# Performance work log

Hardware: AMD Instinct MI355X
Metric: run time of the kernel (lower is better)

## Reference

```python
import jax, jax.numpy as jnp
import numpy as np

B, D, C = 4096, 4096, 1024


def setup_inputs() -> dict:
    key = jax.random.key(0)
    kx, kw = jax.random.split(key)
    x = jax.random.normal(kx, (B, D), dtype=jnp.float32)
    # kaiming_normal_ with nonlinearity='relu': std = sqrt(2 / fan_in)
    W = jax.random.normal(kw, (C, D), dtype=jnp.float32) * jnp.sqrt(2.0 / D)
    return {"x": x, "W": W}


def reference(x, W):
    # Original: -( (x[:, :, None] - W.T[None, :, :])**2 ).mean(axis=1)
    d = x.shape[1]
    x_sq = jnp.sum(x * x, axis=1, keepdims=True)        # [B, 1]
    w_sq = jnp.sum(W * W, axis=1)[None, :]              # [1, C]
    cross = jnp.einsum('bd,cd->bc', x, W)               # [B, C] tensor-core GEMM
    return -(x_sq - 2.0 * cross + w_sq) / d
```

## Files before the change

### kernel.cpp

```cpp
#include <hip/hip_runtime.h>
#include <hip/hip_bf16.h>


typedef float f32x4 __attribute__((ext_vector_type(4)));
typedef float f32x2 __attribute__((ext_vector_type(2)));
typedef long long2_t __attribute__((ext_vector_type(2)));

#define BDIM 4096
#define DDIM 4096
#define CDIM 1024
#define TM 128
#define TN 128
#define BK 64
#define KSPLIT 4
#define NIT ((DDIM / KSPLIT) / BK)
#define SCALE 32.0f
#define INV_SS (1.0f/1024.0f)
#define PSCALE 0.0625f

#define SYNC_LGKM() asm volatile("s_waitcnt lgkmcnt(0)\n\ts_barrier" ::: "memory")

__global__ __launch_bounds__(256) void cvt_rowsq(
    const float* __restrict__ x, const float* __restrict__ W,
    unsigned char* __restrict__ xb, unsigned char* __restrict__ wb,
    float* __restrict__ xsq, float* __restrict__ wsq)
{
    const int lane = threadIdx.x & 63;
    const int row = blockIdx.x * 4 + (threadIdx.x >> 6);

    const float* src;
    unsigned char* dst;
    float* sq;
    if (row < BDIM) {
        src = x + (size_t)row * DDIM;
        dst = xb + (size_t)row * DDIM;
        sq = xsq + row;
    } else {
        int r = row - BDIM;
        src = W + (size_t)r * DDIM;
        dst = wb + (size_t)r * DDIM;
        sq = wsq + r;
    }

    const float4* s4 = (const float4*)src;
    unsigned int* d4 = (unsigned int*)dst;
    float a = 0.f;
    #pragma unroll
    for (int s = 0; s < DDIM / 4 / 64; ++s) {
        float4 f = s4[lane + 64 * s];
        a += f.x * f.x + f.y * f.y + f.z * f.z + f.w * f.w;
        unsigned int p = 0;
        p = __builtin_amdgcn_cvt_pk_fp8_f32(f.x * SCALE, f.y * SCALE, p, false);
        p = __builtin_amdgcn_cvt_pk_fp8_f32(f.z * SCALE, f.w * SCALE, p, true);
        d4[lane + 64 * s] = p;
    }
    #pragma unroll
    for (int off = 32; off > 0; off >>= 1) a += __shfl_down(a, off);
    if (lane == 0) *sq = a;
}

struct Pref { long2_t a0, a1, b0, b1; };

__global__ __launch_bounds__(256, 3) void gemm_eucl(
    const unsigned char* __restrict__ xb,
    const unsigned char* __restrict__ wb,
    unsigned int* __restrict__ part)
{
    __shared__ unsigned char sm[2 * 16384];

    const int tid = threadIdx.x;
    const int lane = tid & 63;
    const int wid = tid >> 6;
    const int bm = blockIdx.x * TM;
    const int bn = blockIdx.y * TN;
    const int ks = blockIdx.z * (DDIM / KSPLIT);
    const int wm = (wid >> 1) * 64;
    const int wn = (wid & 1) * 64;

    const int r0 = tid >> 2, c = tid & 3;
    const unsigned int oA0 = (unsigned int)((bm + r0) * DDIM + ks + c * 16);
    const unsigned int oA1 = oA0 + 64u * DDIM;
    const unsigned int oB0 = (unsigned int)((bn + r0) * DDIM + ks + c * 16);
    const unsigned int oB1 = oB0 + 64u * DDIM;

    const int k2o = (c >> 1) * 8;
    const int kcw = (c & 1) * 2;
    const int wo0 = r0 * 64 + ((kcw ^ (r0 & 3)) * 16) + k2o;
    const int wo1 = r0 * 64 + (((kcw | 1) ^ (r0 & 3)) * 16) + k2o;

    const int kc = lane >> 4;
    const int ml = lane & 15;
    int aoff[4], boff[4];
    #pragma unroll
    for (int i = 0; i < 4; ++i) {
        int m = wm + i * 16 + ml;
        aoff[i] = m * 64 + ((kc ^ (m & 3)) * 16);
        int n = wn + i * 16 + ml;
        boff[i] = n * 64 + ((kc ^ (n & 3)) * 16);
    }

    f32x4 acc[4][4] = {};

#define LOADSET(S, KT)                                                   \
    do {                                                                 \
        (S).a0 = *(const long2_t*)(xb + oA0 + (KT) * BK);                \
        (S).a1 = *(const long2_t*)(xb + oA1 + (KT) * BK);                \
        (S).b0 = *(const long2_t*)(wb + oB0 + (KT) * BK);                \
        (S).b1 = *(const long2_t*)(wb + oB1 + (KT) * BK);                \
    } while (0)

#define WRITESET(buf, S)                                                 \
    do {                                                                 \
        unsigned char* sA = sm + (buf) * 16384;                          \
        unsigned char* sB = sA + 8192;                                   \
        *(long*)(sA + wo0) = (S).a0.x; *(long*)(sA + wo1) = (S).a0.y;    \
        *(long*)(sA + wo0 + 4096) = (S).a1.x;                            \
        *(long*)(sA + wo1 + 4096) = (S).a1.y;                            \
        *(long*)(sB + wo0) = (S).b0.x; *(long*)(sB + wo1) = (S).b0.y;    \
        *(long*)(sB + wo0 + 4096) = (S).b1.x;                            \
        *(long*)(sB + wo1 + 4096) = (S).b1.y;                            \
    } while (0)

#define MFMA8(LA, I)                                                     \
    do {                                                                 \
        _Pragma("unroll")                                                \
        for (int j = 0; j < 4; ++j) {                                    \
            acc[I][j] = __builtin_amdgcn_mfma_f32_16x16x32_fp8_fp8(      \
                (LA).x, lb[j].x, acc[I][j], 0, 0, 0);                    \
            acc[I][j] = __builtin_amdgcn_mfma_f32_16x16x32_fp8_fp8(      \
                (LA).y, lb[j].y, acc[I][j], 0, 0, 0);                    \
        }                                                                \
    } while (0)

#define COMPUTE(buf)                                                     \
    do {                                                                 \
        const unsigned char* sA = sm + (buf) * 16384;                    \
        const unsigned char* sB = sA + 8192;                             \
        long2_t lb[4];                                                   \
        _Pragma("unroll")                                                \
        for (int j = 0; j < 4; ++j) lb[j] = *(const long2_t*)(sB + boff[j]); \
        long2_t laA = *(const long2_t*)(sA + aoff[0]);                   \
        long2_t laB = *(const long2_t*)(sA + aoff[1]);                   \
        MFMA8(laA, 0);                                                   \
        laA = *(const long2_t*)(sA + aoff[2]);                           \
        MFMA8(laB, 1);                                                   \
        laB = *(const long2_t*)(sA + aoff[3]);                           \
        MFMA8(laA, 2);                                                   \
        MFMA8(laB, 3);                                                   \
    } while (0)

    Pref S[3];
    LOADSET(S[0], 0);
    LOADSET(S[1], 1);
    LOADSET(S[2], 2);
    WRITESET(0, S[0]);
    SYNC_LGKM();

    #pragma unroll
    for (int k = 0; k < NIT - 1; ++k) {
        if (k < NIT - 3) LOADSET(S[k % 3], k + 3);
        COMPUTE(k & 1);
        WRITESET((k + 1) & 1, S[(k + 1) % 3]);
        SYNC_LGKM();
    }
    COMPUTE((NIT - 1) & 1);

    unsigned int* p = part
        + (((size_t)blockIdx.z * 256 + (blockIdx.x * 8 + blockIdx.y)) * 16) * 256;
    #pragma unroll
    for (int i = 0; i < 4; ++i)
        #pragma unroll
        for (int j = 0; j < 4; ++j) {
            unsigned int pk = 0;
            pk = __builtin_amdgcn_cvt_pk_fp8_f32(
                acc[i][j][0] * PSCALE, acc[i][j][1] * PSCALE, pk, false);
            pk = __builtin_amdgcn_cvt_pk_fp8_f32(
                acc[i][j][2] * PSCALE, acc[i][j][3] * PSCALE, pk, true);
            p[(i * 4 + j) * 256 + tid] = pk;
        }
#undef LOADSET
#undef WRITESET
#undef MFMA8
#undef COMPUTE
}

__global__ __launch_bounds__(256) void reduce_out(
    const unsigned int* __restrict__ part, const float* __restrict__ xsq,
    const float* __restrict__ wsq, float* __restrict__ out)
{
    const int bid = blockIdx.x;
    const int bb = bid >> 1;
    const int f0 = (bid & 1) * 8;
    const int t = threadIdx.x;
    const int lane = t & 63;
    const int wid = t >> 6;
    const int bm = (bb >> 3) * TM, bn = (bb & 7) * TN;
    const int wm = (wid >> 1) * 64, wn = (wid & 1) * 64;
    const int row_l = (lane >> 4) * 4, col_l = lane & 15;
    const size_t sl = (size_t)256 * 16 * 256;
    const float c1 = 2.0f * 16.0f * INV_SS / (float)DDIM;
    const float c2 = 1.0f / (float)DDIM;

    #pragma unroll
    for (int f = f0; f < f0 + 8; ++f) {
        size_t o = ((size_t)bb * 16 + f) * 256 + t;
        f32x2 s01 = {0.f, 0.f}, s23 = {0.f, 0.f};
        #pragma unroll
        for (int z = 0; z < KSPLIT; ++z) {
            unsigned int u = part[o + (size_t)z * sl];
            s01 += __builtin_amdgcn_cvt_pk_f32_fp8(u, false);
            s23 += __builtin_amdgcn_cvt_pk_f32_fp8(u, true);
        }
        int i = f >> 2, j = f & 3;
        int gn = bn + wn + j * 16 + col_l;
        float wv = wsq[gn];
        float sv[4] = {s01.x, s01.y, s23.x, s23.y};
        #pragma unroll
        for (int r = 0; r < 4; ++r) {
            int gm = bm + wm + i * 16 + row_l + r;
            out[(size_t)gm * CDIM + gn] = sv[r] * c1 - (xsq[gm] + wv) * c2;
        }
    }
}

__global__ void fallback_kernel(const float* __restrict__ x, const float* __restrict__ W,
                                float* __restrict__ out)
{
    int c = blockIdx.x * blockDim.x + threadIdx.x;
    int b = blockIdx.y;
    if (c >= CDIM) return;
    const float* xr = x + (size_t)b * DDIM;
    const float* wr = W + (size_t)c * DDIM;
    float xs = 0.f, ws = 0.f, cr = 0.f;
    for (int d = 0; d < DDIM; ++d) {
        float xv = xr[d], wv = wr[d];
        xs += xv * xv; ws += wv * wv; cr += xv * wv;
    }
    out[(size_t)b * CDIM + c] = (2.0f * cr - xs - ws) / (float)DDIM;
}

extern "C" void kernel_launch(void* const* d_in, const int* in_sizes, int n_in,
                              void* d_out, int out_size, void* d_ws, size_t ws_size,
                              hipStream_t stream) {
    const float* x = (const float*)d_in[0];
    const float* W = (const float*)d_in[1];
    float* out = (float*)d_out;

    size_t need = (size_t)(BDIM + CDIM) * DDIM
                + (size_t)(BDIM + CDIM) * sizeof(float)
                + (size_t)KSPLIT * BDIM * CDIM;
    if (ws_size < need) {
        fallback_kernel<<<dim3(CDIM / 256, BDIM), 256, 0, stream>>>(x, W, out);
        return;
    }

    unsigned char* xb = (unsigned char*)d_ws;
    unsigned char* wb = xb + (size_t)BDIM * DDIM;
    float* xsq = (float*)(wb + (size_t)CDIM * DDIM);
    float* wsq = xsq + BDIM;
    unsigned int* part = (unsigned int*)(wsq + CDIM);

    cvt_rowsq<<<(BDIM + CDIM) / 4, 256, 0, stream>>>(x, W, xb, wb, xsq, wsq);
    gemm_eucl<<<dim3(BDIM / TM, CDIM / TN, KSPLIT), 256, 0, stream>>>(xb, wb, part);
    reduce_out<<<512, 256, 0, stream>>>(part, xsq, wsq, out);
}
```

Baseline: 144.2 us.

## Switch FP8 GEMM to 32x32x64 scaled MFMA with new LDS swizzle

Replaces the 16x16x32 fp8 MFMA pairs with the MI355X 32x32x64 f8f6f4 scaled MFMA, using unit scales. Each wave now computes four 32x32 tiles. LDS writes become single 16-byte stores under a new XOR swizzle, and fragment reads are paired 16-byte loads. The output layout in the partial buffer changes, and the reduction kernel's index mapping is updated to match. The aim is fewer MFMA issues and LDS instructions per K step, at the cost of possible bank conflicts or register pressure under the new layout.

```diff
diff --git a/kernel.cpp b/kernel.cpp
--- a/kernel.cpp
+++ b/kernel.cpp
@@ -4,7 +4,9 @@
 
 typedef float f32x4 __attribute__((ext_vector_type(4)));
 typedef float f32x2 __attribute__((ext_vector_type(2)));
-typedef long long2_t __attribute__((ext_vector_type(2)));
+typedef float f32x16 __attribute__((ext_vector_type(16)));
+typedef int i32x4 __attribute__((ext_vector_type(4)));
+typedef int i32x8 __attribute__((ext_vector_type(8)));
 
 #define BDIM 4096
 #define DDIM 4096
@@ -59,7 +61,18 @@
     if (lane == 0) *sq = a;
 }
 
-struct Pref { long2_t a0, a1, b0, b1; };
+struct Pref { i32x4 a0, a1, b0, b1; };
+
+__device__ __forceinline__ i32x8 rd8(const unsigned char* p0,
+                                     const unsigned char* p1) {
+    i32x4 lo = *(const i32x4*)p0;
+    i32x4 hi = *(const i32x4*)p1;
+    return __builtin_shufflevector(lo, hi, 0, 1, 2, 3, 4, 5, 6, 7);
+}
+
+#define MXMFMA(A, Bv, C)                                                  \
+    __builtin_amdgcn_mfma_scale_f32_32x32x64_f8f6f4(                      \
+        (A), (Bv), (C), 0, 0, 0, 0x7F7F7F7F, 0, 0x7F7F7F7F)
 
 __global__ __launch_bounds__(256, 3) void gemm_eucl(
     const unsigned char* __restrict__ xb,
@@ -83,70 +96,49 @@
     const unsigned int oB0 = (unsigned int)((bn + r0) * DDIM + ks + c * 16);
     const unsigned int oB1 = oB0 + 64u * DDIM;
 
-    const int k2o = (c >> 1) * 8;
-    const int kcw = (c & 1) * 2;
-    const int wo0 = r0 * 64 + ((kcw ^ (r0 & 3)) * 16) + k2o;
-    const int wo1 = r0 * 64 + (((kcw | 1) ^ (r0 & 3)) * 16) + k2o;
-
-    const int kc = lane >> 4;
-    const int ml = lane & 15;
-    int aoff[4], boff[4];
-    #pragma unroll
-    for (int i = 0; i < 4; ++i) {
-        int m = wm + i * 16 + ml;
-        aoff[i] = m * 64 + ((kc ^ (m & 3)) * 16);
-        int n = wn + i * 16 + ml;
-        boff[i] = n * 64 + ((kc ^ (n & 3)) * 16);
-    }
-
-    f32x4 acc[4][4] = {};
+    const int wo0 = r0 * 64 + ((c ^ ((r0 >> 1) & 3)) * 16);
+
+    const int sswz = (lane >> 1) & 3;
+    const int c0 = (lane >> 5) * 2;
+    const int m0 = wm + (lane & 31);
+    const int n0 = wn + (lane & 31);
+    const int aof0 = m0 * 64 + ((c0 ^ sswz) * 16);
+    const int aof1 = m0 * 64 + (((c0 + 1) ^ sswz) * 16);
+    const int bof0 = n0 * 64 + ((c0 ^ sswz) * 16);
+    const int bof1 = n0 * 64 + (((c0 + 1) ^ sswz) * 16);
+
+    f32x16 acc[4] = {};
 
 #define LOADSET(S, KT)                                                   \
     do {                                                                 \
-        (S).a0 = *(const long2_t*)(xb + oA0 + (KT) * BK);                \
-        (S).a1 = *(const long2_t*)(xb + oA1 + (KT) * BK);                \
-        (S).b0 = *(const long2_t*)(wb + oB0 + (KT) * BK);                \
-        (S).b1 = *(const long2_t*)(wb + oB1 + (KT) * BK);                \
+        (S).a0 = *(const i32x4*)(xb + oA0 + (KT) * BK);                  \
+        (S).a1 = *(const i32x4*)(xb + oA1 + (KT) * BK);                  \
+        (S).b0 = *(const i32x4*)(wb + oB0 + (KT) * BK);                  \
+        (S).b1 = *(const i32x4*)(wb + oB1 + (KT) * BK);                  \
     } while (0)
 
 #define WRITESET(buf, S)                                                 \
     do {                                                                 \
         unsigned char* sA = sm + (buf) * 16384;                          \
         unsigned char* sB = sA + 8192;                                   \
-        *(long*)(sA + wo0) = (S).a0.x; *(long*)(sA + wo1) = (S).a0.y;    \
-        *(long*)(sA + wo0 + 4096) = (S).a1.x;                            \
-        *(long*)(sA + wo1 + 4096) = (S).a1.y;                            \
-        *(long*)(sB + wo0) = (S).b0.x; *(long*)(sB + wo1) = (S).b0.y;    \
-        *(long*)(sB + wo0 + 4096) = (S).b1.x;                            \
-        *(long*)(sB + wo1 + 4096) = (S).b1.y;                            \
-    } while (0)
-
-#define MFMA8(LA, I)                                                     \
-    do {                                                                 \
-        _Pragma("unroll")                                                \
-        for (int j = 0; j < 4; ++j) {                                    \
-            acc[I][j] = __builtin_amdgcn_mfma_f32_16x16x32_fp8_fp8(      \
-                (LA).x, lb[j].x, acc[I][j], 0, 0, 0);                    \
-            acc[I][j] = __builtin_amdgcn_mfma_f32_16x16x32_fp8_fp8(      \
-                (LA).y, lb[j].y, acc[I][j], 0, 0, 0);                    \
-        }                                                                \
+        *(i32x4*)(sA + wo0) = (S).a0;                                    \
+        *(i32x4*)(sA + wo0 + 4096) = (S).a1;                             \
+        *(i32x4*)(sB + wo0) = (S).b0;                                    \
+        *(i32x4*)(sB + wo0 + 4096) = (S).b1;                             \
     } while (0)
 
 #define COMPUTE(buf)                                                     \
     do {                                                                 \
         const unsigned char* sA = sm + (buf) * 16384;                    \
         const unsigned char* sB = sA + 8192;                             \
-        long2_t lb[4];                                                   \
-        _Pragma("unroll")                                                \
-        for (int j = 0; j < 4; ++j) lb[j] = *(const long2_t*)(sB + boff[j]); \
-        long2_t laA = *(const long2_t*)(sA + aoff[0]);                   \
-        long2_t laB = *(const long2_t*)(sA + aoff[1]);                   \
-        MFMA8(laA, 0);                                                   \
-        laA = *(const long2_t*)(sA + aoff[2]);                           \
-        MFMA8(laB, 1);                                                   \
-        laB = *(const long2_t*)(sA + aoff[3]);                           \
-        MFMA8(laA, 2);                                                   \
-        MFMA8(laB, 3);                                                   \
+        i32x8 fb0 = rd8(sB + bof0, sB + bof1);                           \
+        i32x8 fb1 = rd8(sB + bof0 + 2048, sB + bof1 + 2048);             \
+        i32x8 fa0 = rd8(sA + aof0, sA + aof1);                           \
+        acc[0] = MXMFMA(fa0, fb0, acc[0]);                               \
+        i32x8 fa1 = rd8(sA + aof0 + 2048, sA + aof1 + 2048);             \
+        acc[1] = MXMFMA(fa0, fb1, acc[1]);                               \
+        acc[2] = MXMFMA(fa1, fb0, acc[2]);                               \
+        acc[3] = MXMFMA(fa1, fb1, acc[3]);                               \
     } while (0)
 
     Pref S[3];
@@ -168,19 +160,18 @@
     unsigned int* p = part
         + (((size_t)blockIdx.z * 256 + (blockIdx.x * 8 + blockIdx.y)) * 16) * 256;
     #pragma unroll
-    for (int i = 0; i < 4; ++i)
+    for (int t = 0; t < 4; ++t)
         #pragma unroll
-        for (int j = 0; j < 4; ++j) {
+        for (int g = 0; g < 4; ++g) {
             unsigned int pk = 0;
             pk = __builtin_amdgcn_cvt_pk_fp8_f32(
-                acc[i][j][0] * PSCALE, acc[i][j][1] * PSCALE, pk, false);
+                acc[t][g * 4 + 0] * PSCALE, acc[t][g * 4 + 1] * PSCALE, pk, false);
             pk = __builtin_amdgcn_cvt_pk_fp8_f32(
-                acc[i][j][2] * PSCALE, acc[i][j][3] * PSCALE, pk, true);
-            p[(i * 4 + j) * 256 + tid] = pk;
+                acc[t][g * 4 + 2] * PSCALE, acc[t][g * 4 + 3] * PSCALE, pk, true);
+            p[(t * 4 + g) * 256 + tid] = pk;
         }
 #undef LOADSET
 #undef WRITESET
-#undef MFMA8
 #undef COMPUTE
 }
 
@@ -196,7 +187,6 @@
     const int wid = t >> 6;
     const int bm = (bb >> 3) * TM, bn = (bb & 7) * TN;
     const int wm = (wid >> 1) * 64, wn = (wid & 1) * 64;
-    const int row_l = (lane >> 4) * 4, col_l = lane & 15;
     const size_t sl = (size_t)256 * 16 * 256;
     const float c1 = 2.0f * 16.0f * INV_SS / (float)DDIM;
     const float c2 = 1.0f / (float)DDIM;
@@ -211,14 +201,15 @@
             s01 += __builtin_amdgcn_cvt_pk_f32_fp8(u, false);
             s23 += __builtin_amdgcn_cvt_pk_f32_fp8(u, true);
         }
-        int i = f >> 2, j = f & 3;
-        int gn = bn + wn + j * 16 + col_l;
+        int t4 = f >> 2, g = f & 3;
+        int it = t4 >> 1, jt = t4 & 1;
+        int gn = bn + wn + jt * 32 + (lane & 31);
         float wv = wsq[gn];
+        int gm0 = bm + wm + it * 32 + (lane >> 5) * 4 + g * 8;
         float sv[4] = {s01.x, s01.y, s23.x, s23.y};
         #pragma unroll
         for (int r = 0; r < 4; ++r) {
-            int gm = bm + wm + i * 16 + row_l + r;
-            out[(size_t)gm * CDIM + gn] = sv[r] * c1 - (xsq[gm] + wv) * c2;
+            out[(size_t)(gm0 + r) * CDIM + gn] = sv[r] * c1 - (xsq[gm0 + r] + wv) * c2;
         }
     }
 }
```

Result: faster. 139.4 us (-3.3%).
